# Optimization experiments

Measured on AMD Instinct MI355X. Metric: run time of the kernel, lower is better.

Reference implementation:

```python
import jax, jax.numpy as jnp
import numpy as np

B, S, E, H = 2, 2048, 2048, 8
D = E // H          # 256, also PMSNorm width
LAYER_IDX = 3
EPS = 1e-5
NEG = jnp.finfo(jnp.float32).min


def setup_inputs() -> dict:
    key = jax.random.key(0)
    k1, k2, k3 = jax.random.split(key, 3)
    return {
        "hidden_state": jax.random.normal(k1, (B, S, E), dtype=jnp.float32),
        "w_attn": jax.random.normal(k2, (E, 3 * E), dtype=jnp.float32) * 0.02,
        "w_proj": jax.random.normal(k3, (E, E), dtype=jnp.float32) * 0.02,
        "norm_weight": jnp.ones((D,), dtype=jnp.float32),
    }


def reference(hidden_state, w_attn, w_proj, norm_weight):
    # qkv projection (Linear, no bias): [B,S,3E]
    qkv = hidden_state @ w_attn
    q, k, v = jnp.split(qkv, 3, axis=-1)
    # split heads -> [B,H,S,D]
    q = q.reshape(B, S, H, D).transpose(0, 2, 1, 3)
    k = k.reshape(B, S, H, D).transpose(0, 2, 1, 3)
    v = v.reshape(B, S, H, D).transpose(0, 2, 1, 3)
    # scaled scores, extra layer-idx scaling as in the module
    scale = jnp.asarray(D, jnp.float32) ** 0.5 * (LAYER_IDX + 1)
    scores = jnp.einsum("bhqd,bhkd->bhqk", q, k) / scale
    # causal mask (tril buffer): masked positions -> float32 min
    causal = jnp.tril(jnp.ones((S, S), dtype=bool))
    scores = jnp.where(causal[None, None], scores, NEG)
    attn = jax.nn.softmax(scores, axis=-1)  # dropout is identity in eval
    o = jnp.einsum("bhqk,bhkd->bhqd", attn, v)
    # PMSNorm over last dim D (applied per-head, as in the source)
    o = o * jax.lax.rsqrt(jnp.mean(o * o, axis=-1, keepdims=True) + EPS)
    o = o * norm_weight
    # merge heads -> [B,S,E], output projection
    merged = o.transpose(0, 2, 1, 3).reshape(B, S, E)
    return merged @ w_proj
```

## Files before the change

kernel.cpp:

```cpp
#include <hip/hip_runtime.h>
#include <math.h>


typedef unsigned short u16;
typedef unsigned int   u32;
typedef u16   u16x8 __attribute__((ext_vector_type(8)));
typedef __bf16 bf16x8 __attribute__((ext_vector_type(8)));
typedef float f32x4 __attribute__((ext_vector_type(4)));

#define GPTR(p) ((const __attribute__((address_space(1))) void*)(p))
#define LPTR(p) ((__attribute__((address_space(3))) void*)(p))

__device__ __forceinline__ u16 f2bf(float x) {
  u32 u = __float_as_uint(x);
  return (u16)((u + 0x7fffu + ((u >> 16) & 1u)) >> 16);
}

__device__ __forceinline__ bf16x8 ld8(const void* p) {
  u16x8 v = *reinterpret_cast<const u16x8*>(p);
  return __builtin_bit_cast(bf16x8, v);
}

__device__ __forceinline__ void g2l16(const void* g, void* l) {
  __builtin_amdgcn_global_load_lds(GPTR(g), LPTR(l), 16, 0, 0);
}

__global__ void cast_bf16_kernel(const float* __restrict__ in, u16* __restrict__ out, int n8) {
  int i = blockIdx.x * 256 + threadIdx.x;
  if (i >= n8) return;
  const float4* p = reinterpret_cast<const float4*>(in) + (size_t)i * 2;
  float4 a = p[0], b = p[1];
  u16x8 v;
  v[0] = f2bf(a.x); v[1] = f2bf(a.y); v[2] = f2bf(a.z); v[3] = f2bf(a.w);
  v[4] = f2bf(b.x); v[5] = f2bf(b.y); v[6] = f2bf(b.z); v[7] = f2bf(b.w);
  reinterpret_cast<u16x8*>(out)[i] = v;
}

__global__ void tcast_kernel(const float* __restrict__ in, u16* __restrict__ out, int R, int C) {
  __shared__ float t[32][33];
  int bx = blockIdx.x * 32, by = blockIdx.y * 32;
  int x = threadIdx.x, y = threadIdx.y;
  #pragma unroll
  for (int k = 0; k < 32; k += 8)
    t[y + k][x] = in[(size_t)(by + y + k) * C + (bx + x)];
  __syncthreads();
  #pragma unroll
  for (int k = 0; k < 32; k += 8)
    out[(size_t)(bx + y + k) * R + (by + x)] = f2bf(t[x][y + k]);
}

__global__ void tv_kernel(const u16* __restrict__ qkv, u16* __restrict__ out) {
  __shared__ u16 t[32][33];
  int bh = blockIdx.z, b = bh >> 3, h = bh & 7;
  const u16* ip = qkv + (size_t)b * 2048 * 6144 + 4096 + h * 256;
  u16* op = out + (size_t)bh * 256 * 2048;
  int bx = blockIdx.x * 32, by = blockIdx.y * 32;
  int x = threadIdx.x, y = threadIdx.y;
  #pragma unroll
  for (int k = 0; k < 32; k += 8)
    t[y + k][x] = ip[(size_t)(by + y + k) * 6144 + (bx + x)];
  __syncthreads();
  #pragma unroll
  for (int k = 0; k < 32; k += 8)
    op[(size_t)(bx + y + k) * 2048 + (by + x)] = t[x][y + k];
}

template<int WM, int WN, int MF, int NF, bool F32OUT>
__global__ __launch_bounds__(512, 4) void gemm2b_kernel(
    const u16* __restrict__ A, const u16* __restrict__ Bt,
    float* __restrict__ Cf, u16* __restrict__ Cb, int M, int N, int K) {
  constexpr int BM = WM * MF * 16;
  constexpr int BN = WN * NF * 16;
  constexpr int TILEB = (BM + BN) * 128;
  constexpr int NSTG = TILEB / 8192;
  __shared__ __align__(16) char smem[2 * TILEB];

  const int tid = threadIdx.x, lane = tid & 63, w = tid >> 6;
  const int wr = w / WN, wc = w % WN;
  const int g = lane >> 4, li = lane & 15;
  const int bn = blockIdx.x * BN, bm = blockIdx.y * BM;

  const char* src[NSTG]; u32 dOff[NSTG];
  #pragma unroll
  for (int j = 0; j < NSTG; ++j) {
    int o = j * 8192 + tid * 16;
    if (o < BM * 128) {
      int row = o >> 7;
      int col = (o & 127) ^ ((row & 7) << 4);
      src[j] = (const char*)A + (size_t)(bm + row) * K * 2 + col;
    } else {
      int rem = o - BM * 128;
      int row = rem >> 7;
      int col = (rem & 127) ^ ((row & 7) << 4);
      src[j] = (const char*)Bt + (size_t)(bn + row) * K * 2 + col;
    }
    dOff[j] = (u32)(o - lane * 16);
  }

  u32 aRd[2][MF], bRd[2][NF];
  #pragma unroll
  for (int ks = 0; ks < 2; ++ks) {
    #pragma unroll
    for (int mf = 0; mf < MF; ++mf) {
      int row = wr * (MF * 16) + mf * 16 + li;
      aRd[ks][mf] = row * 128 + ((ks * 64 + g * 16) ^ ((row & 7) << 4));
    }
    #pragma unroll
    for (int nf = 0; nf < NF; ++nf) {
      int row = wc * (NF * 16) + nf * 16 + li;
      bRd[ks][nf] = BM * 128 + row * 128 + ((ks * 64 + g * 16) ^ ((row & 7) << 4));
    }
  }

  const f32x4 fz = {0.f, 0.f, 0.f, 0.f};
  f32x4 acc[MF][NF];
  #pragma unroll
  for (int i = 0; i < MF; ++i)
    #pragma unroll
    for (int j = 0; j < NF; ++j) acc[i][j] = fz;

  const int NT = K >> 6;
  #pragma unroll
  for (int j = 0; j < NSTG; ++j) { g2l16(src[j], smem + dOff[j]); src[j] += 128; }

  for (int t = 0; t < NT; ++t) {
    const int cur = t & 1;
    const bool more = (t + 1 < NT);
    asm volatile("s_barrier" ::: "memory");
    if (more) {
      char* nb = smem + (cur ^ 1) * TILEB;
      #pragma unroll
      for (int j = 0; j < NSTG; ++j) { g2l16(src[j], nb + dOff[j]); src[j] += 128; }
      asm volatile("s_waitcnt vmcnt(%0)" :: "i"(NSTG) : "memory");
    } else {
      asm volatile("s_waitcnt vmcnt(0)" ::: "memory");
    }
    asm volatile("s_barrier" ::: "memory");

    const char* sb = smem + cur * TILEB;
    #pragma unroll
    for (int ks = 0; ks < 2; ++ks) {
      bf16x8 aR[MF], bR[NF];
      #pragma unroll
      for (int mf = 0; mf < MF; ++mf) aR[mf] = ld8(sb + aRd[ks][mf]);
      #pragma unroll
      for (int nf = 0; nf < NF; ++nf) bR[nf] = ld8(sb + bRd[ks][nf]);
      __builtin_amdgcn_s_setprio(1);
      #pragma unroll
      for (int mf = 0; mf < MF; ++mf)
        #pragma unroll
        for (int nf = 0; nf < NF; ++nf)
          acc[mf][nf] = __builtin_amdgcn_mfma_f32_16x16x32_bf16(aR[mf], bR[nf], acc[mf][nf], 0, 0, 0);
      __builtin_amdgcn_s_setprio(0);
    }
  }

  #pragma unroll
  for (int mf = 0; mf < MF; ++mf)
    #pragma unroll
    for (int nf = 0; nf < NF; ++nf)
      #pragma unroll
      for (int r = 0; r < 4; ++r) {
        int gm = bm + wr * (MF * 16) + mf * 16 + g * 4 + r;
        int gn = bn + wc * (NF * 16) + nf * 16 + li;
        if (F32OUT) Cf[(size_t)gm * N + gn] = acc[mf][nf][r];
        else        Cb[(size_t)gm * N + gn] = f2bf(acc[mf][nf][r]);
      }
}

__global__ __launch_bounds__(512, 2) void attn_kernel(
    const u16* __restrict__ qkv, const u16* __restrict__ Vt,
    const float* __restrict__ nw, u16* __restrict__ Mrg) {
  __shared__ __align__(16) char smem[106496];
  char* sKb = smem;
  char* sVb = smem + 65536;
  char* sPb = smem + 65536 + 32768;
  float* oex  = (float*)smem;
  float* mlex = (float*)(smem + 65536);

  const int c = blockIdx.x;
  const int bh = c & 15, iu = c >> 4;
  const int b = bh >> 3, h = bh & 7;
  const int tid = threadIdx.x, lane = tid & 63, w = tid >> 6;
  const int kh = w >> 2, wq = w & 3;
  const int g = lane >> 4, li = lane & 15;
  const float MASKV = -30000.0f;
  const float MINIT = -1000.0f;
  const float isc = 1.0f / 64.0f;
  const f32x4 fz = {0.f, 0.f, 0.f, 0.f};
  const size_t KADV = (size_t)32 * 6144 * 2;

  #pragma unroll 1
  for (int uu = 0; uu < 2; ++uu) {
    const int qt = uu ? (31 - iu) : iu;
    const int nt = qt + 1;
    const int kvb0 = kh * nt * 32;

    int qrow = qt * 64 + wq * 16 + li;
    const u16* qp = qkv + (size_t)(b * 2048 + qrow) * 6144 + h * 256;
    bf16x8 qf[8];
    #pragma unroll
    for (int c8 = 0; c8 < 8; ++c8) qf[c8] = ld8(qp + c8 * 32 + g * 8);

    const char* kSrc[4]; u32 kDoff[4];
    #pragma unroll
    for (int j = 0; j < 4; ++j) {
      int chunk = wq * 4 + j;
      int o = chunk * 1024 + lane * 16;
      int row = o >> 9, cb = o & 511;
      int cbs = cb ^ ((row & 7) << 4);
      kSrc[j] = (const char*)qkv + ((size_t)(b * 2048 + kvb0 + row) * 6144 + 2048 + h * 256) * 2 + cbs;
      kDoff[j] = chunk * 1024;
    }
    const char* vSrc[4]; char* vDst[4];
    #pragma unroll
    for (int j = 0; j < 4; ++j) {
      int chunk = wq * 4 + j;
      int o = chunk * 1024 + lane * 16;
      int row = o >> 6, cb = o & 63;
      int cbs = cb ^ (((row >> 1) & 3) << 4);
      vSrc[j] = (const char*)Vt + ((size_t)(bh * 256 + row) * 2048 + kvb0) * 2 + cbs;
      vDst[j] = sVb + kh * 16384 + chunk * 1024;
    }

    f32x4 o_[16];
    #pragma unroll
    for (int nf = 0; nf < 16; ++nf) o_[nf] = fz;
    float m_[4] = {MINIT, MINIT, MINIT, MINIT};
    float l_[4] = {0.f, 0.f, 0.f, 0.f};

    {
      char* kb0 = sKb + (kh * 2 + 0) * 16384;
      #pragma unroll
      for (int j = 0; j < 4; ++j) { g2l16(kSrc[j], kb0 + kDoff[j]); kSrc[j] += KADV; }
    }
    asm volatile("s_waitcnt vmcnt(0)" ::: "memory");
    asm volatile("s_barrier" ::: "memory");

    int cur = 0;
    for (int t = 0; t < nt; ++t) {
      const bool more = (t < nt - 1);
      #pragma unroll
      for (int j = 0; j < 4; ++j) { g2l16(vSrc[j], vDst[j]); vSrc[j] += 64; }
      if (more) {
        char* kb = sKb + (kh * 2 + (cur ^ 1)) * 16384;
        #pragma unroll
        for (int j = 0; j < 4; ++j) { g2l16(kSrc[j], kb + kDoff[j]); kSrc[j] += KADV; }
      }

      f32x4 sacc[2];
      const char* kbase = sKb + (kh * 2 + cur) * 16384;
      __builtin_amdgcn_s_setprio(1);
      #pragma unroll
      for (int nf = 0; nf < 2; ++nf) {
        int row = nf * 16 + li;
        int swz = (row & 7) << 4;
        const char* kr = kbase + row * 512;
        f32x4 sa = fz, sb = fz;
        #pragma unroll
        for (int c8 = 0; c8 < 4; ++c8) {
          sa = __builtin_amdgcn_mfma_f32_16x16x32_bf16(qf[c8],     ld8(kr + ((c8 * 64 + g * 16) ^ swz)),       sa, 0, 0, 0);
          sb = __builtin_amdgcn_mfma_f32_16x16x32_bf16(qf[c8 + 4], ld8(kr + (((c8 + 4) * 64 + g * 16) ^ swz)), sb, 0, 0, 0);
        }
        sacc[nf] = sa + sb;
      }
      __builtin_amdgcn_s_setprio(0);

      const int tidx = kh * nt + t;
      const bool diag = (tidx >= 2 * qt);
      float p[2][4], m0[4];
      #pragma unroll
      for (int r = 0; r < 4; ++r) {
        int qr = qt * 64 + wq * 16 + g * 4 + r;
        float a0 = sacc[0][r] * isc;
        float a1 = sacc[1][r] * isc;
        if (diag) {
          if (tidx * 32 + li > qr) a0 = MASKV;
          if (tidx * 32 + 16 + li > qr) a1 = MASKV;
        }
        p[0][r] = a0; p[1][r] = a1;
        m0[r] = fmaxf(a0, a1);
      }
      bool need = (m0[0] > m_[0] + 8.f) || (m0[1] > m_[1] + 8.f) ||
                  (m0[2] > m_[2] + 8.f) || (m0[3] > m_[3] + 8.f);
      if (__any(need)) {
        #pragma unroll
        for (int r = 0; r < 4; ++r) {
          float mx = m0[r];
          mx = fmaxf(mx, __shfl_xor(mx, 1));
          mx = fmaxf(mx, __shfl_xor(mx, 2));
          mx = fmaxf(mx, __shfl_xor(mx, 4));
          mx = fmaxf(mx, __shfl_xor(mx, 8));
          float mn = fmaxf(m_[r], mx);
          float sc = __expf(m_[r] - mn);
          l_[r] *= sc; m_[r] = mn;
          #pragma unroll
          for (int nf = 0; nf < 16; ++nf) o_[nf][r] *= sc;
        }
      }
      #pragma unroll
      for (int r = 0; r < 4; ++r) {
        float e0 = __expf(p[0][r] - m_[r]);
        float e1 = __expf(p[1][r] - m_[r]);
        p[0][r] = e0; p[1][r] = e1;
        l_[r] += e0 + e1;
      }

      if (more) asm volatile("s_waitcnt vmcnt(4)" ::: "memory");
      else      asm volatile("s_waitcnt vmcnt(0)" ::: "memory");
      asm volatile("s_barrier" ::: "memory");

      char* sPw = sPb + kh * 4096 + wq * 1024;
      #pragma unroll
      for (int r = 0; r < 4; ++r) {
        int row = g * 4 + r;
        int swz = ((row >> 1) & 3) << 4;
        #pragma unroll
        for (int nf = 0; nf < 2; ++nf)
          *(u16*)(sPw + row * 64 + (((nf * 16 + li) * 2) ^ swz)) = f2bf(p[nf][r]);
      }
      asm volatile("s_waitcnt lgkmcnt(0)" ::: "memory");
      __builtin_amdgcn_sched_barrier(0);

      __builtin_amdgcn_s_setprio(1);
      {
        const char* vb = sVb + kh * 16384;
        bf16x8 pa = ld8(sPw + li * 64 + ((g * 16) ^ (((li >> 1) & 3) << 4)));
        #pragma unroll
        for (int nf = 0; nf < 16; ++nf) {
          int row = nf * 16 + li;
          bf16x8 vf = ld8(vb + row * 64 + ((g * 16) ^ (((row >> 1) & 3) << 4)));
          o_[nf] = __builtin_amdgcn_mfma_f32_16x16x32_bf16(pa, vf, o_[nf], 0, 0, 0);
        }
      }
      __builtin_amdgcn_s_setprio(0);

      asm volatile("s_barrier" ::: "memory");
      if (more) asm volatile("s_waitcnt vmcnt(0)" ::: "memory");
      cur ^= 1;
    }

    if (kh == 1) {
      #pragma unroll
      for (int nf = 0; nf < 16; ++nf)
        *(f32x4*)(oex + wq * 4096 + nf * 256 + lane * 4) = o_[nf];
      #pragma unroll
      for (int r = 0; r < 4; ++r) {
        mlex[wq * 512 + r * 64 + lane] = l_[r];
        mlex[wq * 512 + 256 + r * 64 + lane] = m_[r];
      }
    }
    __syncthreads();
    if (kh == 0) {
      float aw[4], bw[4], inv_l[4];
      #pragma unroll
      for (int r = 0; r < 4; ++r) {
        float mB = mlex[wq * 512 + 256 + r * 64 + lane];
        float lB = mlex[wq * 512 + r * 64 + lane];
        float mm = fmaxf(m_[r], mB);
        aw[r] = __expf(m_[r] - mm);
        bw[r] = __expf(mB - mm);
        float lr = l_[r] * aw[r] + lB * bw[r];
        lr += __shfl_xor(lr, 1);
        lr += __shfl_xor(lr, 2);
        lr += __shfl_xor(lr, 4);
        lr += __shfl_xor(lr, 8);
        inv_l[r] = 1.0f / lr;
      }
      #pragma unroll
      for (int nf = 0; nf < 16; ++nf) {
        f32x4 ob = *(f32x4*)(oex + wq * 4096 + nf * 256 + lane * 4);
        #pragma unroll
        for (int r = 0; r < 4; ++r)
          o_[nf][r] = o_[nf][r] * aw[r] + ob[r] * bw[r];
      }
      #pragma unroll
      for (int r = 0; r < 4; ++r) {
        float ss = 0.f;
        #pragma unroll
        for (int nf = 0; nf < 16; ++nf) {
          float v = o_[nf][r] * inv_l[r];
          ss += v * v;
        }
        ss += __shfl_xor(ss, 1);
        ss += __shfl_xor(ss, 2);
        ss += __shfl_xor(ss, 4);
        ss += __shfl_xor(ss, 8);
        float rms = rsqrtf(ss * (1.0f / 256.0f) + 1e-5f);
        int row = qt * 64 + wq * 16 + g * 4 + r;
        #pragma unroll
        for (int nf = 0; nf < 16; ++nf) {
          int d = nf * 16 + li;
          float v = o_[nf][r] * inv_l[r] * rms * nw[d];
          Mrg[((size_t)(b * 2048 + row)) * 2048 + h * 256 + d] = f2bf(v);
        }
      }
    }
    __syncthreads();
  }
}

extern "C" void kernel_launch(void* const* d_in, const int* in_sizes, int n_in,
                              void* d_out, int out_size, void* d_ws, size_t ws_size,
                              hipStream_t stream) {
  const float* hs  = (const float*)d_in[0];
  const float* wat = (const float*)d_in[1];
  const float* wpr = (const float*)d_in[2];
  const float* nw  = (const float*)d_in[3];
  float* out = (float*)d_out;

  char* ws = (char*)d_ws;
  u16* Xb   = (u16*)(ws + 0);
  u16* Wp_t = (u16*)(ws + (16u << 20));
  u16* Qkv  = (u16*)(ws + (24u << 20));
  u16* Vt   = (u16*)(ws + (72u << 20));
  u16* Mrg  = Xb;
  u16* Wa_t = (u16*)d_out;

  dim3 t328(32, 8);
  cast_bf16_kernel<<<4096, 256, 0, stream>>>(hs, Xb, 1048576);
  tcast_kernel<<<dim3(192, 64), t328, 0, stream>>>(wat, Wa_t, 2048, 6144);
  tcast_kernel<<<dim3(64, 64), t328, 0, stream>>>(wpr, Wp_t, 2048, 2048);
  gemm2b_kernel<2, 4, 4, 3, false><<<dim3(32, 32), 512, 0, stream>>>(
      Xb, Wa_t, nullptr, Qkv, 4096, 6144, 2048);
  tv_kernel<<<dim3(8, 64, 16), t328, 0, stream>>>(Qkv, Vt);
  attn_kernel<<<256, 512, 0, stream>>>(Qkv, Vt, nw, Mrg);
  gemm2b_kernel<2, 4, 4, 2, true><<<dim3(16, 32), 512, 0, stream>>>(
      Mrg, Wp_t, out, nullptr, 4096, 2048, 2048);
  (void)in_sizes; (void)n_in; (void)out_size; (void)ws_size;
}
```

Before: 237.4 us.

## Fuse cast/transpose prep kernels and add 4-stage pipelined QKV GEMM

```diff
diff --git a/kernel.cpp b/kernel.cpp
--- a/kernel.cpp
+++ b/kernel.cpp
@@ -25,21 +25,32 @@
   __builtin_amdgcn_global_load_lds(GPTR(g), LPTR(l), 16, 0, 0);
 }
 
-__global__ void cast_bf16_kernel(const float* __restrict__ in, u16* __restrict__ out, int n8) {
-  int i = blockIdx.x * 256 + threadIdx.x;
-  if (i >= n8) return;
-  const float4* p = reinterpret_cast<const float4*>(in) + (size_t)i * 2;
-  float4 a = p[0], b = p[1];
-  u16x8 v;
-  v[0] = f2bf(a.x); v[1] = f2bf(a.y); v[2] = f2bf(a.z); v[3] = f2bf(a.w);
-  v[4] = f2bf(b.x); v[5] = f2bf(b.y); v[6] = f2bf(b.z); v[7] = f2bf(b.w);
-  reinterpret_cast<u16x8*>(out)[i] = v;
-}
-
-__global__ void tcast_kernel(const float* __restrict__ in, u16* __restrict__ out, int R, int C) {
+__global__ void prep_kernel(const float* __restrict__ hs, const float* __restrict__ wat,
+                            const float* __restrict__ wpr, u16* __restrict__ Xb,
+                            u16* __restrict__ Wa_t, u16* __restrict__ Wp_t) {
   __shared__ float t[32][33];
-  int bx = blockIdx.x * 32, by = blockIdx.y * 32;
-  int x = threadIdx.x, y = threadIdx.y;
+  const int bid = blockIdx.x, tid = threadIdx.x;
+  if (bid < 4096) {
+    int i = bid * 256 + tid;
+    const float4* p = reinterpret_cast<const float4*>(hs) + (size_t)i * 2;
+    float4 a = p[0], b = p[1];
+    u16x8 v;
+    v[0] = f2bf(a.x); v[1] = f2bf(a.y); v[2] = f2bf(a.z); v[3] = f2bf(a.w);
+    v[4] = f2bf(b.x); v[5] = f2bf(b.y); v[6] = f2bf(b.z); v[7] = f2bf(b.w);
+    reinterpret_cast<u16x8*>(Xb)[i] = v;
+    return;
+  }
+  const float* in; u16* out; int R, C, bx, by;
+  if (bid < 16384) {
+    int b2 = bid - 4096;
+    in = wat; out = Wa_t; R = 2048; C = 6144;
+    bx = (b2 % 192) * 32; by = (b2 / 192) * 32;
+  } else {
+    int b3 = bid - 16384;
+    in = wpr; out = Wp_t; R = 2048; C = 2048;
+    bx = (b3 % 64) * 32; by = (b3 / 64) * 32;
+  }
+  int x = tid & 31, y = tid >> 5;
   #pragma unroll
   for (int k = 0; k < 32; k += 8)
     t[y + k][x] = in[(size_t)(by + y + k) * C + (bx + x)];
@@ -63,6 +74,105 @@
   #pragma unroll
   for (int k = 0; k < 32; k += 8)
     op[(size_t)(bx + y + k) * 2048 + (by + x)] = t[x][y + k];
+}
+
+template<int WM, int WN, int MF, int NF>
+__global__ __launch_bounds__(512, 4) void gemm4d_kernel(
+    const u16* __restrict__ A, const u16* __restrict__ Bt,
+    u16* __restrict__ Cb, int M, int N, int K) {
+  constexpr int BM = WM * MF * 16;
+  constexpr int BN = WN * NF * 16;
+  constexpr int TILEB = (BM + BN) * 64;
+  constexpr int NSTG = TILEB / 8192;
+  __shared__ __align__(16) char smem[4 * TILEB];
+
+  const int tid = threadIdx.x, lane = tid & 63, w = tid >> 6;
+  const int wr = w / WN, wc = w % WN;
+  const int g = lane >> 4, li = lane & 15;
+  const int bn = blockIdx.x * BN, bm = blockIdx.y * BM;
+
+  const char* src[NSTG]; u32 dOff[NSTG];
+  #pragma unroll
+  for (int j = 0; j < NSTG; ++j) {
+    int o = j * 8192 + tid * 16;
+    if (o < BM * 64) {
+      int row = o >> 6;
+      int col = (o & 63) ^ (((row >> 1) & 3) << 4);
+      src[j] = (const char*)A + (size_t)(bm + row) * K * 2 + col;
+    } else {
+      int rem = o - BM * 64;
+      int row = rem >> 6;
+      int col = (rem & 63) ^ (((row >> 1) & 3) << 4);
+      src[j] = (const char*)Bt + (size_t)(bn + row) * K * 2 + col;
+    }
+    dOff[j] = (u32)(o - lane * 16);
+  }
+
+  u32 aRd[MF], bRd[NF];
+  #pragma unroll
+  for (int mf = 0; mf < MF; ++mf) {
+    int row = wr * (MF * 16) + mf * 16 + li;
+    aRd[mf] = row * 64 + ((g * 16) ^ (((row >> 1) & 3) << 4));
+  }
+  #pragma unroll
+  for (int nf = 0; nf < NF; ++nf) {
+    int row = wc * (NF * 16) + nf * 16 + li;
+    bRd[nf] = BM * 64 + row * 64 + ((g * 16) ^ (((row >> 1) & 3) << 4));
+  }
+
+  const f32x4 fz = {0.f, 0.f, 0.f, 0.f};
+  f32x4 acc[MF][NF];
+  #pragma unroll
+  for (int i = 0; i < MF; ++i)
+    #pragma unroll
+    for (int j = 0; j < NF; ++j) acc[i][j] = fz;
+
+  const int NT = K >> 5;
+  #pragma unroll
+  for (int tt = 0; tt < 3; ++tt)
+    #pragma unroll
+    for (int j = 0; j < NSTG; ++j) { g2l16(src[j], smem + tt * TILEB + dOff[j]); src[j] += 64; }
+
+  for (int t = 0; t < NT; ++t) {
+    asm volatile("s_barrier" ::: "memory");
+    if (t + 3 < NT) {
+      char* nb = smem + ((t + 3) & 3) * TILEB;
+      #pragma unroll
+      for (int j = 0; j < NSTG; ++j) { g2l16(src[j], nb + dOff[j]); src[j] += 64; }
+      asm volatile("s_waitcnt vmcnt(6)" ::: "memory");
+    } else {
+      int rem = NT - 1 - t;
+      if (rem == 2)      asm volatile("s_waitcnt vmcnt(4)" ::: "memory");
+      else if (rem == 1) asm volatile("s_waitcnt vmcnt(2)" ::: "memory");
+      else               asm volatile("s_waitcnt vmcnt(0)" ::: "memory");
+    }
+    asm volatile("s_barrier" ::: "memory");
+
+    const char* sb = smem + (t & 3) * TILEB;
+    bf16x8 aR[MF], bR[NF];
+    #pragma unroll
+    for (int mf = 0; mf < MF; ++mf) aR[mf] = ld8(sb + aRd[mf]);
+    #pragma unroll
+    for (int nf = 0; nf < NF; ++nf) bR[nf] = ld8(sb + bRd[nf]);
+    __builtin_amdgcn_s_setprio(1);
+    #pragma unroll
+    for (int mf = 0; mf < MF; ++mf)
+      #pragma unroll
+      for (int nf = 0; nf < NF; ++nf)
+        acc[mf][nf] = __builtin_amdgcn_mfma_f32_16x16x32_bf16(aR[mf], bR[nf], acc[mf][nf], 0, 0, 0);
+    __builtin_amdgcn_s_setprio(0);
+  }
+
+  #pragma unroll
+  for (int mf = 0; mf < MF; ++mf)
+    #pragma unroll
+    for (int nf = 0; nf < NF; ++nf)
+      #pragma unroll
+      for (int r = 0; r < 4; ++r) {
+        int gm = bm + wr * (MF * 16) + mf * 16 + g * 4 + r;
+        int gn = bn + wc * (NF * 16) + nf * 16 + li;
+        Cb[(size_t)gm * N + gn] = f2bf(acc[mf][nf][r]);
+      }
 }
 
 template<int WM, int WN, int MF, int NF, bool F32OUT>
@@ -418,11 +528,9 @@
   u16* Wa_t = (u16*)d_out;
 
   dim3 t328(32, 8);
-  cast_bf16_kernel<<<4096, 256, 0, stream>>>(hs, Xb, 1048576);
-  tcast_kernel<<<dim3(192, 64), t328, 0, stream>>>(wat, Wa_t, 2048, 6144);
-  tcast_kernel<<<dim3(64, 64), t328, 0, stream>>>(wpr, Wp_t, 2048, 2048);
-  gemm2b_kernel<2, 4, 4, 3, false><<<dim3(32, 32), 512, 0, stream>>>(
-      Xb, Wa_t, nullptr, Qkv, 4096, 6144, 2048);
+  prep_kernel<<<20480, 256, 0, stream>>>(hs, wat, wpr, Xb, Wa_t, Wp_t);
+  gemm4d_kernel<2, 4, 4, 2><<<dim3(48, 32), 512, 0, stream>>>(
+      Xb, Wa_t, Qkv, 4096, 6144, 2048);
   tv_kernel<<<dim3(8, 64, 16), t328, 0, stream>>>(Qkv, Vt);
   attn_kernel<<<256, 512, 0, stream>>>(Qkv, Vt, nw, Mrg);
   gemm2b_kernel<2, 4, 4, 2, true><<<dim3(16, 32), 512, 0, stream>>>(
```

Measured after the change: 257.3 us. 1.08x slower.

## Merge input cast/transpose kernels into one launch and remap GEMM blocks per XCD

Applied to the files above, without the earlier changes.

```diff
diff --git a/kernel.cpp b/kernel.cpp
--- a/kernel.cpp
+++ b/kernel.cpp
@@ -25,21 +25,32 @@
   __builtin_amdgcn_global_load_lds(GPTR(g), LPTR(l), 16, 0, 0);
 }
 
-__global__ void cast_bf16_kernel(const float* __restrict__ in, u16* __restrict__ out, int n8) {
-  int i = blockIdx.x * 256 + threadIdx.x;
-  if (i >= n8) return;
-  const float4* p = reinterpret_cast<const float4*>(in) + (size_t)i * 2;
-  float4 a = p[0], b = p[1];
-  u16x8 v;
-  v[0] = f2bf(a.x); v[1] = f2bf(a.y); v[2] = f2bf(a.z); v[3] = f2bf(a.w);
-  v[4] = f2bf(b.x); v[5] = f2bf(b.y); v[6] = f2bf(b.z); v[7] = f2bf(b.w);
-  reinterpret_cast<u16x8*>(out)[i] = v;
-}
-
-__global__ void tcast_kernel(const float* __restrict__ in, u16* __restrict__ out, int R, int C) {
+__global__ void prep_kernel(const float* __restrict__ hs, const float* __restrict__ wat,
+                            const float* __restrict__ wpr, u16* __restrict__ Xb,
+                            u16* __restrict__ Wa_t, u16* __restrict__ Wp_t) {
   __shared__ float t[32][33];
-  int bx = blockIdx.x * 32, by = blockIdx.y * 32;
-  int x = threadIdx.x, y = threadIdx.y;
+  const int bid = blockIdx.x, tid = threadIdx.x;
+  if (bid < 4096) {
+    int i = bid * 256 + tid;
+    const float4* p = reinterpret_cast<const float4*>(hs) + (size_t)i * 2;
+    float4 a = p[0], b = p[1];
+    u16x8 v;
+    v[0] = f2bf(a.x); v[1] = f2bf(a.y); v[2] = f2bf(a.z); v[3] = f2bf(a.w);
+    v[4] = f2bf(b.x); v[5] = f2bf(b.y); v[6] = f2bf(b.z); v[7] = f2bf(b.w);
+    reinterpret_cast<u16x8*>(Xb)[i] = v;
+    return;
+  }
+  const float* in; u16* out; int R, C, bx, by;
+  if (bid < 16384) {
+    int b2 = bid - 4096;
+    in = wat; out = Wa_t; R = 2048; C = 6144;
+    bx = (b2 % 192) * 32; by = (b2 / 192) * 32;
+  } else {
+    int b3 = bid - 16384;
+    in = wpr; out = Wp_t; R = 2048; C = 2048;
+    bx = (b3 % 64) * 32; by = (b3 / 64) * 32;
+  }
+  int x = tid & 31, y = tid >> 5;
   #pragma unroll
   for (int k = 0; k < 32; k += 8)
     t[y + k][x] = in[(size_t)(by + y + k) * C + (bx + x)];
@@ -78,7 +89,13 @@
   const int tid = threadIdx.x, lane = tid & 63, w = tid >> 6;
   const int wr = w / WN, wc = w % WN;
   const int g = lane >> 4, li = lane & 15;
-  const int bn = blockIdx.x * BN, bm = blockIdx.y * BM;
+
+  const int gx = gridDim.x;
+  const int nwg = gx * gridDim.y;
+  const int bid = blockIdx.y * gx + blockIdx.x;
+  const int cpx = nwg >> 3;
+  const int wu = (bid & 7) * cpx + (bid >> 3);
+  const int bn = (wu % gx) * BN, bm = (wu / gx) * BM;
 
   const char* src[NSTG]; u32 dOff[NSTG];
   #pragma unroll
@@ -418,9 +435,7 @@
   u16* Wa_t = (u16*)d_out;
 
   dim3 t328(32, 8);
-  cast_bf16_kernel<<<4096, 256, 0, stream>>>(hs, Xb, 1048576);
-  tcast_kernel<<<dim3(192, 64), t328, 0, stream>>>(wat, Wa_t, 2048, 6144);
-  tcast_kernel<<<dim3(64, 64), t328, 0, stream>>>(wpr, Wp_t, 2048, 2048);
+  prep_kernel<<<20480, 256, 0, stream>>>(hs, wat, wpr, Xb, Wa_t, Wp_t);
   gemm2b_kernel<2, 4, 4, 3, false><<<dim3(32, 32), 512, 0, stream>>>(
       Xb, Wa_t, nullptr, Qkv, 4096, 6144, 2048);
   tv_kernel<<<dim3(8, 64, 16), t328, 0, stream>>>(Qkv, Vt);
```

Measured after the change: 260.1 us. +9.6%, slower.
